# Kernel tuning notes

Hardware: AMD Instinct MI355X
Metric: run time of the kernel (lower is better)

Reference implementation:

```python
import jax, jax.numpy as jnp
import numpy as np
from jax import lax

FILTERS = 64

def _conv(a, k):
    # NHWC input, HWIO kernel, SAME padding, stride 1
    return lax.conv_general_dilated(a, k, window_strides=(1, 1), padding='SAME',
                                    dimension_numbers=('NHWC', 'HWIO', 'NHWC'))

def _hard_sigmoid(z):
    # Keras ConvLSTM2D default recurrent_activation
    return jnp.clip(0.2 * z + 0.5, 0.0, 1.0)

def setup_inputs() -> dict:
    key = jax.random.key(0)
    k1, k2, k3 = jax.random.split(key, 3)
    B, T, H, W, C = 8, 16, 96, 96, 8
    x = jax.random.normal(k1, (B, T, H, W, C), dtype=jnp.float32)
    Wx = jax.random.normal(k2, (3, 3, C, 4 * FILTERS), dtype=jnp.float32) * 0.05
    Wh = jax.random.normal(k3, (3, 3, FILTERS, 4 * FILTERS), dtype=jnp.float32) * 0.05
    b = jnp.zeros((4 * FILTERS,), dtype=jnp.float32)
    return {"x": x, "Wx": Wx, "Wh": Wh, "b": b}

def reference(x, Wx, Wh, b):
    # Keras ConvLSTM2D forward (inference: dropout off), return_sequences=False.
    B, T, H, W, C = x.shape
    F = Wh.shape[2]

    def step(carry, xt):
        h, c = carry
        z = _conv(xt, Wx) + _conv(h, Wh) + b  # (B,H,W,4F)
        i, f, g, o = jnp.split(z, 4, axis=-1)  # Keras gate order i,f,c,o
        i = _hard_sigmoid(i)
        f = _hard_sigmoid(f)
        o = _hard_sigmoid(o)
        c_new = f * c + i * jnp.tanh(g)
        h_new = o * jnp.tanh(c_new)
        return (h_new, c_new), None

    h0 = jnp.zeros((B, H, W, F), x.dtype)
    xs = jnp.moveaxis(x, 1, 0)  # (T,B,H,W,C)
    (h, c), _ = lax.scan(step, (h0, h0), xs)
    return h  # (B,H,W,F)
```

## Files before the change

### kernel.cpp

```cpp
#include <hip/hip_runtime.h>
#include <cmath>


#define HTOT 96
#define WTOT 96
#define CINX 8
#define FF   64
#define G4   256
#define BB   8
#define TT   16
#define NPOS (BB*HTOT*WTOT)

typedef __attribute__((ext_vector_type(8))) short short8;
typedef __attribute__((ext_vector_type(4))) float floatx4;

union U16 { uint4 u; short8 s; };

__device__ __forceinline__ float hsig(float z) {
    return fminf(fmaxf(0.2f * z + 0.5f, 0.f), 1.f);
}

__device__ __forceinline__ float ftanh(float x) {
    float e = __expf(-2.f * fabsf(x));
    float t = (1.f - e) / (1.f + e);
    return copysignf(t, x);
}

__device__ __forceinline__ ushort f2bf(float f) {
    unsigned u = __float_as_uint(f);
    u = (u + 0x7fff + ((u >> 16) & 1)) >> 16;
    return (ushort)u;
}

__device__ __forceinline__ void async16(const void* g, void* l) {
    __builtin_amdgcn_global_load_lds(
        (const __attribute__((address_space(1))) void*)g,
        (__attribute__((address_space(3))) void*)l, 16, 0, 0);
}

__global__ __launch_bounds__(256) void conv_x_bf16(const float* __restrict__ x,
                                                   ushort* __restrict__ xbf, int n4) {
    int i = blockIdx.x * 256 + threadIdx.x;
    if (i >= n4) return;
    float4 v = ((const float4*)x)[i];
    ushort4 o;
    o.x = f2bf(v.x); o.y = f2bf(v.y); o.z = f2bf(v.z); o.w = f2bf(v.w);
    ((ushort4*)xbf)[i] = o;
}

__global__ __launch_bounds__(256) void prep_w(const float* __restrict__ Wx,
                                              const float* __restrict__ Wh,
                                              ushort* __restrict__ Bp) {
    int idx = blockIdx.x * 256 + threadIdx.x;
    if (idx >= 4 * 21 * 256) return;
    int lane = idx & 63;
    int g = (idx >> 6) & 3;
    int rest = idx >> 8;
    int s = rest % 21, slice = rest / 21;
    int q = lane >> 4, col = lane & 15;
    int n = g * 64 + slice * 16 + col;
    ushort o[8];
    if (s < 18) {
        int dxw = s / 6, rem = s - 6 * dxw;
        int khw = rem / 3, dyw = rem - 3 * khw;
        int tap = dyw * 3 + dxw;
        int cbase = khw * 32 + q * 8;
        #pragma unroll
        for (int j = 0; j < 8; ++j)
            o[j] = f2bf(Wh[((size_t)tap * FF + cbase + j) * G4 + n]);
    } else {
        int tap = (s - 18) * 4 + q;
        #pragma unroll
        for (int j = 0; j < 8; ++j)
            o[j] = (tap < 9) ? f2bf(Wx[((size_t)tap * CINX + j) * G4 + n]) : (ushort)0;
    }
    U16 u;
    #pragma unroll
    for (int j = 0; j < 8; ++j) ((ushort*)&u)[j] = o[j];
    ((uint4*)Bp)[idx] = u.u;
}

__global__ __launch_bounds__(256, 4) void convlstm_mfma(
    const ushort* __restrict__ xbf, int t,
    const ushort* __restrict__ hS_in,
    ushort* __restrict__ hS_out,
    float* __restrict__ cS,
    const ushort* __restrict__ Bp,
    const float* __restrict__ bias,
    const uint4* __restrict__ zpad,
    float* __restrict__ out, int last)
{
    __shared__ __align__(16) ushort hplanes[8 * 2048];
    __shared__ __align__(16) ushort xplane[2048];

    const int tid = threadIdx.x;
    const int x0 = blockIdx.x * 16, y0 = blockIdx.y * 12;
    const int bb = blockIdx.z >> 2, slice = blockIdx.z & 3;

    const int w = tid >> 6, lane = tid & 63, q = lane >> 4, col = lane & 15;
    const int rowb = w * 3;

    const uint4* gB = (const uint4*)Bp + (size_t)(slice * 21) * 256 + lane;

    {
        int py = tid / 18, px = tid - py * 18;
        int gy = y0 - 1 + py, gx = x0 - 1 + px;
        bool ok = (gy >= 0 && gy < HTOT && gx >= 0 && gx < WTOT);
        int gyc = gy < 0 ? 0 : (gy > HTOT - 1 ? HTOT - 1 : gy);
        int gxc = gx < 0 ? 0 : (gx > WTOT - 1 ? WTOT - 1 : gx);
        size_t gpos = ((size_t)bb * HTOT + gyc) * WTOT + gxc;
        #pragma unroll
        for (int p = 0; p < 8; ++p) {
            const void* src = ok
                ? (const void*)(hS_in + ((size_t)(p >> 1) * NPOS + gpos) * 16 + (p & 1) * 8)
                : (const void*)zpad;
            async16(src, hplanes + p * 2048 + tid * 8);
        }
        const void* sxp = ok
            ? (const void*)(xbf + ((((size_t)bb * TT + t) * HTOT + gyc) * WTOT + gxc) * CINX)
            : (const void*)zpad;
        async16(sxp, xplane + tid * 8);
    }

    const ushort* hA = hplanes + q * 2048 + (rowb * 18 + col) * 8;

    U16 bbuf[2][4];
    #pragma unroll
    for (int g = 0; g < 4; ++g) bbuf[0][g].u = gB[g * 64];

    floatx4 acc[3][4];
    #pragma unroll
    for (int g = 0; g < 4; ++g) {
        float bv = bias[g * 64 + slice * 16 + col];
        acc[0][g] = (floatx4){bv, bv, bv, bv};
        acc[1][g] = (floatx4){bv, bv, bv, bv};
        acc[2][g] = (floatx4){bv, bv, bv, bv};
    }

    __syncthreads();

    U16 aw[4];
    #pragma unroll
    for (int dx = 0; dx < 3; ++dx) {
        #pragma unroll
        for (int kh = 0; kh < 2; ++kh) {
            #pragma unroll
            for (int j = 0; j < 3; ++j)
                aw[j].u = *(const uint4*)(hA + kh * 8192 + j * 144 + dx * 8);
            #pragma unroll
            for (int dy = 0; dy < 3; ++dy) {
                const int s = dx * 6 + kh * 3 + dy;
                #pragma unroll
                for (int g = 0; g < 4; ++g)
                    bbuf[(s + 1) & 1][g].u = gB[(s + 1) * 256 + g * 64];
                if (dy)
                    aw[(dy + 2) & 3].u = *(const uint4*)(hA + kh * 8192 + (dy + 2) * 144 + dx * 8);
                #pragma unroll
                for (int g = 0; g < 4; ++g)
                    #pragma unroll
                    for (int mt = 0; mt < 3; ++mt)
                        acc[mt][g] = __builtin_amdgcn_mfma_f32_16x16x32_bf16(
                            aw[(mt + dy) & 3].s, bbuf[s & 1][g].s, acc[mt][g], 0, 0, 0);
            }
        }
    }
    #pragma unroll
    for (int sx = 0; sx < 3; ++sx) {
        const int s = 18 + sx;
        int tap = sx * 4 + q; if (tap > 8) tap = 8;
        int dyq = tap / 3, dxq = tap - 3 * dyq;
        const ushort* xA = xplane + ((rowb + dyq) * 18 + col + dxq) * 8;
        if (sx < 2) {
            #pragma unroll
            for (int g = 0; g < 4; ++g)
                bbuf[(s + 1) & 1][g].u = gB[(s + 1) * 256 + g * 64];
        }
        U16 a4[3];
        #pragma unroll
        for (int mt = 0; mt < 3; ++mt)
            a4[mt].u = *(const uint4*)(xA + mt * 144);
        #pragma unroll
        for (int g = 0; g < 4; ++g)
            #pragma unroll
            for (int mt = 0; mt < 3; ++mt)
                acc[mt][g] = __builtin_amdgcn_mfma_f32_16x16x32_bf16(
                    a4[mt].s, bbuf[s & 1][g].s, acc[mt][g], 0, 0, 0);
    }

    #pragma unroll
    for (int mt = 0; mt < 3; ++mt) {
        int gy = y0 + rowb + mt;
        #pragma unroll
        for (int r = 0; r < 4; ++r) {
            int gx = x0 + q * 4 + r;
            size_t gpos = ((size_t)bb * HTOT + gy) * WTOT + gx;
            size_t idx = ((size_t)slice * NPOS + gpos) * 16 + col;
            float zi = acc[mt][0][r], zf = acc[mt][1][r];
            float zg = acc[mt][2][r], zo = acc[mt][3][r];
            float cn = hsig(zf) * cS[idx] + hsig(zi) * ftanh(zg);
            cS[idx] = cn;
            float hn = hsig(zo) * ftanh(cn);
            hS_out[idx] = f2bf(hn);
            if (last) out[gpos * 64 + slice * 16 + col] = hn;
        }
    }
}

extern "C" void kernel_launch(void* const* d_in, const int* in_sizes, int n_in,
                              void* d_out, int out_size, void* d_ws, size_t ws_size,
                              hipStream_t stream) {
    const float* x  = (const float*)d_in[0];
    const float* Wx = (const float*)d_in[1];
    const float* Wh = (const float*)d_in[2];
    const float* b  = (const float*)d_in[3];

    const size_t NX = (size_t)BB * TT * HTOT * WTOT * CINX;
    const size_t NH = (size_t)NPOS * FF;

    char* ws = (char*)d_ws;
    ushort* xbf = (ushort*)ws;                  ws += NX * 2;
    ushort* hS0 = (ushort*)ws;                  ws += NH * 2;
    ushort* hS1 = (ushort*)ws;                  ws += NH * 2;
    float*  cS  = (float*)ws;                   ws += NH * 4;
    ushort* Bp  = (ushort*)ws;                  ws += (size_t)4*21*256*16;
    uint4*  zpad = (uint4*)ws;

    hipMemsetAsync(hS0, 0, NH * 2, stream);
    hipMemsetAsync(cS,  0, NH * 4, stream);
    hipMemsetAsync(zpad, 0, 64, stream);

    conv_x_bf16<<<(int)((NX / 4 + 255) / 256), 256, 0, stream>>>(x, xbf, (int)(NX / 4));
    prep_w<<<(4 * 21 * 256 + 255) / 256, 256, 0, stream>>>(Wx, Wh, Bp);

    dim3 grid(WTOT / 16, HTOT / 12, BB * 4);
    for (int t = 0; t < TT; ++t) {
        const ushort* hin = (t & 1) ? hS1 : hS0;
        ushort* hout      = (t & 1) ? hS0 : hS1;
        convlstm_mfma<<<grid, 256, 0, stream>>>(xbf, t, hin, hout, cS, Bp, b, zpad,
                                                (float*)d_out, t == TT - 1);
    }
}
```

Baseline: 588.3 us.

## Drop LDS staging, load conv operands directly from global, double rows per wave

The step kernel no longer stages the h and x halo tiles in shared memory through async global-to-LDS loads and a barrier. Each wave now reads its A fragments straight from global memory, with per-lane bounds checks that fall back to a zero pad. The tile height doubles to 24 rows, so each wave handles 6 rows and reuses every weight fragment across twice as many MFMAs, while the weight double-buffer is replaced by per-step loads. This halves the grid and raises register pressure (24 accumulators, launch bounds lowered to 3). It relies on L1/L2 to absorb the overlapping halo reads.

New measurement: 653.9 us. 11.1% more time.

```diff
diff --git a/kernel.cpp b/kernel.cpp
--- a/kernel.cpp
+++ b/kernel.cpp
@@ -30,12 +30,6 @@
     unsigned u = __float_as_uint(f);
     u = (u + 0x7fff + ((u >> 16) & 1)) >> 16;
     return (ushort)u;
-}
-
-__device__ __forceinline__ void async16(const void* g, void* l) {
-    __builtin_amdgcn_global_load_lds(
-        (const __attribute__((address_space(1))) void*)g,
-        (__attribute__((address_space(3))) void*)l, 16, 0, 0);
 }
 
 __global__ __launch_bounds__(256) void conv_x_bf16(const float* __restrict__ x,
@@ -80,7 +74,7 @@
     ((uint4*)Bp)[idx] = u.u;
 }
 
-__global__ __launch_bounds__(256, 4) void convlstm_mfma(
+__global__ __launch_bounds__(256, 3) void convlstm_mfma(
     const ushort* __restrict__ xbf, int t,
     const ushort* __restrict__ hS_in,
     ushort* __restrict__ hS_out,
@@ -90,105 +84,90 @@
     const uint4* __restrict__ zpad,
     float* __restrict__ out, int last)
 {
-    __shared__ __align__(16) ushort hplanes[8 * 2048];
-    __shared__ __align__(16) ushort xplane[2048];
-
     const int tid = threadIdx.x;
-    const int x0 = blockIdx.x * 16, y0 = blockIdx.y * 12;
+    const int x0 = blockIdx.x * 16, y0 = blockIdx.y * 24;
     const int bb = blockIdx.z >> 2, slice = blockIdx.z & 3;
-
     const int w = tid >> 6, lane = tid & 63, q = lane >> 4, col = lane & 15;
-    const int rowb = w * 3;
+    const int rowb = w * 6;
 
     const uint4* gB = (const uint4*)Bp + (size_t)(slice * 21) * 256 + lane;
 
-    {
-        int py = tid / 18, px = tid - py * 18;
-        int gy = y0 - 1 + py, gx = x0 - 1 + px;
-        bool ok = (gy >= 0 && gy < HTOT && gx >= 0 && gx < WTOT);
-        int gyc = gy < 0 ? 0 : (gy > HTOT - 1 ? HTOT - 1 : gy);
-        int gxc = gx < 0 ? 0 : (gx > WTOT - 1 ? WTOT - 1 : gx);
-        size_t gpos = ((size_t)bb * HTOT + gyc) * WTOT + gxc;
-        #pragma unroll
-        for (int p = 0; p < 8; ++p) {
-            const void* src = ok
-                ? (const void*)(hS_in + ((size_t)(p >> 1) * NPOS + gpos) * 16 + (p & 1) * 8)
-                : (const void*)zpad;
-            async16(src, hplanes + p * 2048 + tid * 8);
-        }
-        const void* sxp = ok
-            ? (const void*)(xbf + ((((size_t)bb * TT + t) * HTOT + gyc) * WTOT + gxc) * CINX)
-            : (const void*)zpad;
-        async16(sxp, xplane + tid * 8);
-    }
-
-    const ushort* hA = hplanes + q * 2048 + (rowb * 18 + col) * 8;
-
-    U16 bbuf[2][4];
-    #pragma unroll
-    for (int g = 0; g < 4; ++g) bbuf[0][g].u = gB[g * 64];
-
-    floatx4 acc[3][4];
+    const int gyb = y0 + rowb - 1;
+    const int gxl = x0 - 1 + col;
+    const long hb0 = ((long)(q >> 1) * NPOS) * 16 + (q & 1) * 8
+                   + ((long)(bb * HTOT + gyb) * WTOT + gxl) * 16;
+    const long xb0 = (((long)(bb * TT + t) * HTOT + gyb) * WTOT + gxl) * 8;
+
+    floatx4 acc[6][4];
     #pragma unroll
     for (int g = 0; g < 4; ++g) {
         float bv = bias[g * 64 + slice * 16 + col];
-        acc[0][g] = (floatx4){bv, bv, bv, bv};
-        acc[1][g] = (floatx4){bv, bv, bv, bv};
-        acc[2][g] = (floatx4){bv, bv, bv, bv};
-    }
-
-    __syncthreads();
-
-    U16 aw[4];
+        #pragma unroll
+        for (int mt = 0; mt < 6; ++mt) acc[mt][g] = (floatx4){bv, bv, bv, bv};
+    }
+
+    U16 aw[8];
     #pragma unroll
     for (int dx = 0; dx < 3; ++dx) {
+        const bool okx = ((unsigned)(gxl + dx) < (unsigned)WTOT);
         #pragma unroll
         for (int kh = 0; kh < 2; ++kh) {
             #pragma unroll
-            for (int j = 0; j < 3; ++j)
-                aw[j].u = *(const uint4*)(hA + kh * 8192 + j * 144 + dx * 8);
+            for (int j = 0; j < 6; ++j) {
+                bool ok = okx && ((unsigned)(gyb + j) < (unsigned)HTOT);
+                const ushort* p = hS_in + hb0 + (long)kh * (2L * NPOS * 16)
+                                + j * (WTOT * 16) + dx * 16;
+                aw[j].u = *(ok ? (const uint4*)p : zpad);
+            }
             #pragma unroll
             for (int dy = 0; dy < 3; ++dy) {
                 const int s = dx * 6 + kh * 3 + dy;
+                if (dy) {
+                    const int j = 5 + dy;
+                    bool ok = okx && ((unsigned)(gyb + j) < (unsigned)HTOT);
+                    const ushort* p = hS_in + hb0 + (long)kh * (2L * NPOS * 16)
+                                    + j * (WTOT * 16) + dx * 16;
+                    aw[j].u = *(ok ? (const uint4*)p : zpad);
+                }
+                U16 b4[4];
                 #pragma unroll
-                for (int g = 0; g < 4; ++g)
-                    bbuf[(s + 1) & 1][g].u = gB[(s + 1) * 256 + g * 64];
-                if (dy)
-                    aw[(dy + 2) & 3].u = *(const uint4*)(hA + kh * 8192 + (dy + 2) * 144 + dx * 8);
+                for (int g = 0; g < 4; ++g) b4[g].u = gB[s * 256 + g * 64];
                 #pragma unroll
                 for (int g = 0; g < 4; ++g)
                     #pragma unroll
-                    for (int mt = 0; mt < 3; ++mt)
+                    for (int mt = 0; mt < 6; ++mt)
                         acc[mt][g] = __builtin_amdgcn_mfma_f32_16x16x32_bf16(
-                            aw[(mt + dy) & 3].s, bbuf[s & 1][g].s, acc[mt][g], 0, 0, 0);
+                            aw[mt + dy].s, b4[g].s, acc[mt][g], 0, 0, 0);
             }
         }
     }
+
     #pragma unroll
     for (int sx = 0; sx < 3; ++sx) {
         const int s = 18 + sx;
         int tap = sx * 4 + q; if (tap > 8) tap = 8;
         int dyq = tap / 3, dxq = tap - 3 * dyq;
-        const ushort* xA = xplane + ((rowb + dyq) * 18 + col + dxq) * 8;
-        if (sx < 2) {
-            #pragma unroll
-            for (int g = 0; g < 4; ++g)
-                bbuf[(s + 1) & 1][g].u = gB[(s + 1) * 256 + g * 64];
+        const bool okxq = ((unsigned)(gxl + dxq) < (unsigned)WTOT);
+        U16 b4[4], a4[6];
+        #pragma unroll
+        for (int g = 0; g < 4; ++g) b4[g].u = gB[s * 256 + g * 64];
+        #pragma unroll
+        for (int mt = 0; mt < 6; ++mt) {
+            int jj = mt + dyq;
+            bool ok = okxq && ((unsigned)(gyb + jj) < (unsigned)HTOT);
+            const ushort* p = xbf + xb0 + jj * (WTOT * 8) + dxq * 8;
+            a4[mt].u = *(ok ? (const uint4*)p : zpad);
         }
-        U16 a4[3];
-        #pragma unroll
-        for (int mt = 0; mt < 3; ++mt)
-            a4[mt].u = *(const uint4*)(xA + mt * 144);
         #pragma unroll
         for (int g = 0; g < 4; ++g)
             #pragma unroll
-            for (int mt = 0; mt < 3; ++mt)
+            for (int mt = 0; mt < 6; ++mt)
                 acc[mt][g] = __builtin_amdgcn_mfma_f32_16x16x32_bf16(
-                    a4[mt].s, bbuf[s & 1][g].s, acc[mt][g], 0, 0, 0);
-    }
-
-    #pragma unroll
-    for (int mt = 0; mt < 3; ++mt) {
+                    a4[mt].s, b4[g].s, acc[mt][g], 0, 0, 0);
+    }
+
+    #pragma unroll
+    for (int mt = 0; mt < 6; ++mt) {
         int gy = y0 + rowb + mt;
         #pragma unroll
         for (int r = 0; r < 4; ++r) {
@@ -232,7 +211,7 @@
     conv_x_bf16<<<(int)((NX / 4 + 255) / 256), 256, 0, stream>>>(x, xbf, (int)(NX / 4));
     prep_w<<<(4 * 21 * 256 + 255) / 256, 256, 0, stream>>>(Wx, Wh, Bp);
 
-    dim3 grid(WTOT / 16, HTOT / 12, BB * 4);
+    dim3 grid(WTOT / 16, HTOT / 24, BB * 4);
     for (int t = 0; t < TT; ++t) {
         const ushort* hin = (t & 1) ? hS1 : hS0;
         ushort* hout      = (t & 1) ? hS0 : hS1;
```

## Retile ConvLSTM step so each wave handles one filter slice over a 6-row tile

Applied to the files above, without the earlier changes.

Each block now covers a 16x6 spatial tile for all four filter slices: each wave takes one slice and computes 6 rows, instead of four blocks each loading a 16x12 halo for a single slice. The h halo is loaded into LDS once per block and shared across all slices, which cuts redundant global loads of the hidden state. Accumulators double to 6x4 per wave and occupancy is lowered to 3 blocks. The B-operand double buffering is dropped in favour of loading the weights just before use, which may expose global-load latency.

Result: slower. 733.5 us (+24.7%).

```diff
diff --git a/kernel.cpp b/kernel.cpp
--- a/kernel.cpp
+++ b/kernel.cpp
@@ -10,6 +10,7 @@
 #define BB   8
 #define TT   16
 #define NPOS (BB*HTOT*WTOT)
+#define PSTR 1160
 
 typedef __attribute__((ext_vector_type(8))) short short8;
 typedef __attribute__((ext_vector_type(4))) float floatx4;
@@ -80,7 +81,7 @@
     ((uint4*)Bp)[idx] = u.u;
 }
 
-__global__ __launch_bounds__(256, 4) void convlstm_mfma(
+__global__ __launch_bounds__(256, 3) void convlstm_mfma(
     const ushort* __restrict__ xbf, int t,
     const ushort* __restrict__ hS_in,
     ushort* __restrict__ hS_out,
@@ -90,19 +91,18 @@
     const uint4* __restrict__ zpad,
     float* __restrict__ out, int last)
 {
-    __shared__ __align__(16) ushort hplanes[8 * 2048];
-    __shared__ __align__(16) ushort xplane[2048];
+    __shared__ __align__(16) ushort hplanes[8 * PSTR];
+    __shared__ __align__(16) ushort xplane[144 * 8];
 
     const int tid = threadIdx.x;
-    const int x0 = blockIdx.x * 16, y0 = blockIdx.y * 12;
-    const int bb = blockIdx.z >> 2, slice = blockIdx.z & 3;
-
+    const int x0 = blockIdx.x * 16, y0 = blockIdx.y * 6;
+    const int bb = blockIdx.z;
     const int w = tid >> 6, lane = tid & 63, q = lane >> 4, col = lane & 15;
-    const int rowb = w * 3;
+    const int slice = w;
 
     const uint4* gB = (const uint4*)Bp + (size_t)(slice * 21) * 256 + lane;
 
-    {
+    if (tid < 144) {
         int py = tid / 18, px = tid - py * 18;
         int gy = y0 - 1 + py, gx = x0 - 1 + px;
         bool ok = (gy >= 0 && gy < HTOT && gx >= 0 && gx < WTOT);
@@ -111,85 +111,84 @@
         size_t gpos = ((size_t)bb * HTOT + gyc) * WTOT + gxc;
         #pragma unroll
         for (int p = 0; p < 8; ++p) {
+            int s8 = (p >> 2) * 2 + ((p & 3) >> 1), half = p & 1;
             const void* src = ok
-                ? (const void*)(hS_in + ((size_t)(p >> 1) * NPOS + gpos) * 16 + (p & 1) * 8)
+                ? (const void*)(hS_in + ((size_t)s8 * NPOS + gpos) * 16 + half * 8)
                 : (const void*)zpad;
-            async16(src, hplanes + p * 2048 + tid * 8);
+            async16(src, hplanes + p * PSTR + tid * 8);
         }
-        const void* sxp = ok
+        const void* sx = ok
             ? (const void*)(xbf + ((((size_t)bb * TT + t) * HTOT + gyc) * WTOT + gxc) * CINX)
             : (const void*)zpad;
-        async16(sxp, xplane + tid * 8);
-    }
-
-    const ushort* hA = hplanes + q * 2048 + (rowb * 18 + col) * 8;
-
-    U16 bbuf[2][4];
-    #pragma unroll
-    for (int g = 0; g < 4; ++g) bbuf[0][g].u = gB[g * 64];
-
-    floatx4 acc[3][4];
+        async16(sx, xplane + tid * 8);
+    }
+
+    U16 b4[4];
+    #pragma unroll
+    for (int g = 0; g < 4; ++g) b4[g].u = gB[g * 64];
+
+    floatx4 acc[6][4];
     #pragma unroll
     for (int g = 0; g < 4; ++g) {
         float bv = bias[g * 64 + slice * 16 + col];
-        acc[0][g] = (floatx4){bv, bv, bv, bv};
-        acc[1][g] = (floatx4){bv, bv, bv, bv};
-        acc[2][g] = (floatx4){bv, bv, bv, bv};
+        #pragma unroll
+        for (int mt = 0; mt < 6; ++mt) acc[mt][g] = (floatx4){bv, bv, bv, bv};
     }
 
     __syncthreads();
 
-    U16 aw[4];
+    const ushort* hA = hplanes + q * PSTR + col * 8;
+
+    U16 aw[6];
     #pragma unroll
     for (int dx = 0; dx < 3; ++dx) {
         #pragma unroll
         for (int kh = 0; kh < 2; ++kh) {
             #pragma unroll
-            for (int j = 0; j < 3; ++j)
-                aw[j].u = *(const uint4*)(hA + kh * 8192 + j * 144 + dx * 8);
+            for (int j = 0; j < 6; ++j)
+                aw[j].u = *(const uint4*)(hA + kh * 4 * PSTR + (j * 18 + dx) * 8);
             #pragma unroll
             for (int dy = 0; dy < 3; ++dy) {
                 const int s = dx * 6 + kh * 3 + dy;
-                #pragma unroll
-                for (int g = 0; g < 4; ++g)
-                    bbuf[(s + 1) & 1][g].u = gB[(s + 1) * 256 + g * 64];
                 if (dy)
-                    aw[(dy + 2) & 3].u = *(const uint4*)(hA + kh * 8192 + (dy + 2) * 144 + dx * 8);
+                    aw[(5 + dy) % 6].u =
+                        *(const uint4*)(hA + kh * 4 * PSTR + ((5 + dy) * 18 + dx) * 8);
+                if (s) {
+                    #pragma unroll
+                    for (int g = 0; g < 4; ++g) b4[g].u = gB[s * 256 + g * 64];
+                }
                 #pragma unroll
                 for (int g = 0; g < 4; ++g)
                     #pragma unroll
-                    for (int mt = 0; mt < 3; ++mt)
+                    for (int mt = 0; mt < 6; ++mt)
                         acc[mt][g] = __builtin_amdgcn_mfma_f32_16x16x32_bf16(
-                            aw[(mt + dy) & 3].s, bbuf[s & 1][g].s, acc[mt][g], 0, 0, 0);
+                            aw[(mt + dy) % 6].s, b4[g].s, acc[mt][g], 0, 0, 0);
             }
         }
     }
+
     #pragma unroll
     for (int sx = 0; sx < 3; ++sx) {
         const int s = 18 + sx;
+        #pragma unroll
+        for (int g = 0; g < 4; ++g) b4[g].u = gB[s * 256 + g * 64];
         int tap = sx * 4 + q; if (tap > 8) tap = 8;
         int dyq = tap / 3, dxq = tap - 3 * dyq;
-        const ushort* xA = xplane + ((rowb + dyq) * 18 + col + dxq) * 8;
-        if (sx < 2) {
-            #pragma unroll
-            for (int g = 0; g < 4; ++g)
-                bbuf[(s + 1) & 1][g].u = gB[(s + 1) * 256 + g * 64];
-        }
-        U16 a4[3];
-        #pragma unroll
-        for (int mt = 0; mt < 3; ++mt)
-            a4[mt].u = *(const uint4*)(xA + mt * 144);
+        U16 a4[6];
+        #pragma unroll
+        for (int mt = 0; mt < 6; ++mt)
+            a4[mt].u = *(const uint4*)(xplane + ((mt + dyq) * 18 + col + dxq) * 8);
         #pragma unroll
         for (int g = 0; g < 4; ++g)
             #pragma unroll
-            for (int mt = 0; mt < 3; ++mt)
+            for (int mt = 0; mt < 6; ++mt)
                 acc[mt][g] = __builtin_amdgcn_mfma_f32_16x16x32_bf16(
-                    a4[mt].s, bbuf[s & 1][g].s, acc[mt][g], 0, 0, 0);
-    }
-
-    #pragma unroll
-    for (int mt = 0; mt < 3; ++mt) {
-        int gy = y0 + rowb + mt;
+                    a4[mt].s, b4[g].s, acc[mt][g], 0, 0, 0);
+    }
+
+    #pragma unroll
+    for (int mt = 0; mt < 6; ++mt) {
+        int gy = y0 + mt;
         #pragma unroll
         for (int r = 0; r < 4; ++r) {
             int gx = x0 + q * 4 + r;
@@ -232,7 +231,7 @@
     conv_x_bf16<<<(int)((NX / 4 + 255) / 256), 256, 0, stream>>>(x, xbf, (int)(NX / 4));
     prep_w<<<(4 * 21 * 256 + 255) / 256, 256, 0, stream>>>(Wx, Wh, Bp);
 
-    dim3 grid(WTOT / 16, HTOT / 12, BB * 4);
+    dim3 grid(WTOT / 16, HTOT / 6, BB);
     for (int t = 0; t < TT; ++t) {
         const ushort* hin = (t & 1) ? hS1 : hS0;
         ushort* hout      = (t & 1) ? hS0 : hS1;
```
